# Kernel optimization log

Hardware: AMD Instinct MI355X
Metric: run time of the kernel (lower is better)

## Reference

```python
import jax, jax.numpy as jnp
import numpy as np

EPS = 1e-5
NEG = jnp.float32(-9e15)

def _leaky(z):
    return jnp.where(z >= 0, z, 0.01 * z)

def setup_inputs() -> dict:
    key = jax.random.key(0)
    ks = jax.random.split(key, 12)
    B, N, d_in, d_hid, d_out = 4, 512, 128, 128, 128
    d_mid = d_in // 2
    s = lambda fan: 1.0 / np.sqrt(fan)
    inp = {
        'x': jax.random.normal(ks[0], (B, N, d_in), dtype=jnp.float32),
        'A_init': jax.random.randint(ks[1], (B, N, N), 0, 2, dtype=jnp.int32),
        # Acompute: conv1 (1x1), bn1, conv2 (1x1)
        'W1': jax.random.normal(ks[2], (d_mid, d_in), dtype=jnp.float32) * s(d_in),
        'b1': jnp.zeros((d_mid,), dtype=jnp.float32),
        'g1': jnp.ones((d_mid,), dtype=jnp.float32),
        'be1': jnp.zeros((d_mid,), dtype=jnp.float32),
        'W2': jax.random.normal(ks[3], (1, d_mid), dtype=jnp.float32) * s(d_mid),
        'b2': jnp.zeros((1,), dtype=jnp.float32),
        # Gconv branch1_g0: fc + bn1d
        'Wg': jax.random.normal(ks[4], (d_hid, d_in), dtype=jnp.float32) * s(d_in),
        'bg': jnp.zeros((d_hid,), dtype=jnp.float32),
        'gg': jnp.ones((d_hid,), dtype=jnp.float32),
        'beg': jnp.zeros((d_hid,), dtype=jnp.float32),
        # trans_fc: (d_in + d_hid) -> d_out
        'Wt': jax.random.normal(ks[5], (d_out, d_in + d_hid), dtype=jnp.float32) * s(d_in + d_hid),
        'bt': jnp.zeros((d_out,), dtype=jnp.float32),
    }
    return inp

def reference(x, A_init, W1, b1, g1, be1, W2, b2, Wg, bg, gg, beg, Wt, bt):
    # ---- Acompute: dense pairwise |x_i - x_j| -> 1x1conv -> BN2d -> lrelu -> 1x1conv -> masked softmax
    D = jnp.abs(x[:, :, None, :] - x[:, None, :, :])            # [B, N, N, C]
    h = jnp.einsum('bijc,oc->bijo', D, W1) + b1                 # conv1 (1x1)
    m = jnp.mean(h, axis=(0, 1, 2))                              # BN2d batch stats (training mode)
    v = jnp.mean((h - m) ** 2, axis=(0, 1, 2))                   # biased variance
    h = (h - m) / jnp.sqrt(v + EPS) * g1 + be1
    h = _leaky(h)
    s = jnp.einsum('bijo,uo->biju', h, W2)[..., 0] + b2[0]       # conv2 -> [B, N, N]
    s = jnp.where(A_init > 0, s, NEG)                            # mask non-edges
    A = jax.nn.softmax(s, axis=-1)                               # row-normalized adjacency
    # ---- Gconv branch: bmm -> fc -> BN1d (per-channel over batch*nodes) -> lrelu
    y = jnp.einsum('bij,bjc->bic', A, x)                         # graph aggregation
    y = y @ Wg.T + bg                                            # [B, N, d_hid]
    mg = jnp.mean(y, axis=(0, 1))
    vg = jnp.mean((y - mg) ** 2, axis=(0, 1))
    y = (y - mg) / jnp.sqrt(vg + EPS) * gg + beg
    y = _leaky(y)
    # ---- concat [original, branch1] -> trans_fc
    out = jnp.concatenate([x, y], axis=2) @ Wt.T + bt            # [B, N, d_out]
    return out
```

## Files before the change

### kernel.cpp

```cpp
#include <hip/hip_runtime.h>
#include <hip/hip_bf16.h>
#include <math.h>

#define Bq 4
#define Nq 512
#define Cq 128
#define Oq 64
#define TI 16
#define TJ 8
#define NBLK (Bq*(Nq/TI)*(Nq/TJ))
#define PTOT ((double)Bq*Nq*Nq)
#define NROW (Bq*Nq)
#define EPSq 1e-5f
#define NEGq -9e15f

typedef _Float16 half8 __attribute__((ext_vector_type(8)));
typedef float f32x4 __attribute__((ext_vector_type(4)));

#define OFF_S       0u
#define OFF_YAGG    4194304u
#define OFF_YFC     5242880u
#define OFF_WGT     6291456u
#define OFF_WTT     6356992u
#define OFF_WF      6488064u
#define OFF_PART1   6504448u
#define OFF_RED1    10698752u
#define OFF_SC1     10699776u
#define OFF_PARTG   10700288u
#define OFF_SCG     10962432u
#define WS_NEED     10963456u

__device__ __forceinline__ float lrelu(float v) { return v >= 0.0f ? v : 0.01f * v; }

template <int MODE>
__global__ __launch_bounds__(256, 3) void k_pair_mfma(
    const float* __restrict__ x, const _Float16* __restrict__ Wf,
    const int* __restrict__ A_init, const float* __restrict__ W2,
    const float* __restrict__ b2, const float* __restrict__ scsh,
    float* __restrict__ partial1, float* __restrict__ s_buf) {
  __shared__ float XI[TI][136];
  __shared__ float XJ[TJ][136];
  __shared__ float ep[4][2][64];
  __shared__ float ssc[128];

  const int t = threadIdx.x;
  const int l = t & 63;
  const int wv = __builtin_amdgcn_readfirstlane(t >> 6);
  const int jt = blockIdx.x, it = blockIdx.y, b = blockIdx.z;
  const int i0 = it * TI, j0 = jt * TJ;
  const float* xb = x + (size_t)b * Nq * Cq;

  half8 bf[16];
#pragma unroll
  for (int i = 0; i < 16; ++i)
    bf[i] = *(const half8*)&Wf[(size_t)(i * 64 + l) * 8];

  {
    const int row = t >> 4, col = (t & 15) * 8;
    const float* src = xb + (size_t)(i0 + row) * Cq + col;
    *(float4*)&XI[row][col] = *(const float4*)src;
    *(float4*)&XI[row][col + 4] = *(const float4*)(src + 4);
    if (t < 128) {
      const int rj = t >> 4;
      const float* sj = xb + (size_t)(j0 + rj) * Cq + col;
      *(float4*)&XJ[rj][col] = *(const float4*)sj;
      *(float4*)&XJ[rj][col + 4] = *(const float4*)(sj + 4);
    }
  }
  __syncthreads();

  const int g = l >> 4;
  const int cL = l & 15;
  const int jlan = l & 7;
  const int ilh = (l >> 3) & 1;

  f32x4 zero;
  zero[0] = 0.0f; zero[1] = 0.0f; zero[2] = 0.0f; zero[3] = 0.0f;
  f32x4 acc[2][4];
#pragma unroll
  for (int m = 0; m < 2; ++m)
#pragma unroll
    for (int n = 0; n < 4; ++n) acc[m][n] = zero;

#pragma unroll
  for (int ks = 0; ks < 4; ++ks) {
#pragma unroll
    for (int m = 0; m < 2; ++m) {
      const int mt = wv * 2 + m;
      const int il = mt * 2 + ilh;
      const int c0 = ks * 32 + 4 * g;
      const float4 a0 = *(const float4*)&XI[il][c0];
      const float4 a1 = *(const float4*)&XI[il][c0 + 16];
      const float4 v0 = *(const float4*)&XJ[jlan][c0];
      const float4 v1 = *(const float4*)&XJ[jlan][c0 + 16];
      half8 af;
      af[0] = (_Float16)fabsf(a0.x - v0.x);
      af[1] = (_Float16)fabsf(a0.y - v0.y);
      af[2] = (_Float16)fabsf(a0.z - v0.z);
      af[3] = (_Float16)fabsf(a0.w - v0.w);
      af[4] = (_Float16)fabsf(a1.x - v1.x);
      af[5] = (_Float16)fabsf(a1.y - v1.y);
      af[6] = (_Float16)fabsf(a1.z - v1.z);
      af[7] = (_Float16)fabsf(a1.w - v1.w);
#pragma unroll
      for (int n = 0; n < 4; ++n)
        acc[m][n] = __builtin_amdgcn_mfma_f32_16x16x32_f16(af, bf[ks * 4 + n],
                                                           acc[m][n], 0, 0, 0);
    }
  }

  const int blk = ((b * (Nq / TI) + it) * (Nq / TJ) + jt);

  if (MODE == 0) {
#pragma unroll
    for (int n = 0; n < 4; ++n) {
      float a = 0.0f, q = 0.0f;
#pragma unroll
      for (int m = 0; m < 2; ++m)
#pragma unroll
        for (int r = 0; r < 4; ++r) {
          const float v = acc[m][n][r];
          a += v;
          q += v * v;
        }
      a += __shfl_xor(a, 16); a += __shfl_xor(a, 32);
      q += __shfl_xor(q, 16); q += __shfl_xor(q, 32);
      if (l < 16) {
        ep[wv][0][n * 16 + l] = a;
        ep[wv][1][n * 16 + l] = q;
      }
    }
    __syncthreads();
    if (t < 128) {
      const int o = t & 63, typ = t >> 6;
      const float v = ep[0][typ][o] + ep[1][typ][o] + ep[2][typ][o] + ep[3][typ][o];
      partial1[(size_t)blk * 128 + typ * 64 + o] = v;
    }
    return;
  }

  float sc[4], sh[4], w2[4];
#pragma unroll
  for (int n = 0; n < 4; ++n) {
    const int o = n * 16 + cL;
    sc[n] = scsh[o];
    sh[n] = scsh[64 + o];
    w2[n] = W2[o];
  }
  float sp[2][4];
#pragma unroll
  for (int m = 0; m < 2; ++m)
#pragma unroll
    for (int r = 0; r < 4; ++r) {
      float v = 0.0f;
#pragma unroll
      for (int n = 0; n < 4; ++n) {
        float h = fmaf(acc[m][n][r], sc[n], sh[n]);
        h = lrelu(h);
        v = fmaf(w2[n], h, v);
      }
      v += __shfl_xor(v, 1);
      v += __shfl_xor(v, 2);
      v += __shfl_xor(v, 4);
      v += __shfl_xor(v, 8);
      sp[m][r] = v;
    }
  if (cL == 0) {
#pragma unroll
    for (int m = 0; m < 2; ++m)
#pragma unroll
      for (int r = 0; r < 4; ++r) ssc[wv * 32 + m * 16 + 4 * g + r] = sp[m][r];
  }
  __syncthreads();
  if (t < 128) {
    const int il2 = t >> 3, jl2 = t & 7;
    const size_t arow = ((size_t)b * Nq + (i0 + il2)) * Nq + (j0 + jl2);
    s_buf[arow] = (A_init[arow] > 0) ? ssc[t] + b2[0] : NEGq;
  }
}

__global__ __launch_bounds__(256) void k_reduce1(const float* __restrict__ partial1,
                                                 double* __restrict__ red1) {
  __shared__ double sh[256];
  const int vi = blockIdx.x;
  const int t = threadIdx.x;
  double a = 0.0;
  for (int blk = t; blk < NBLK; blk += 256) a += (double)partial1[(size_t)blk * 128 + vi];
  sh[t] = a;
  __syncthreads();
  for (int off = 128; off > 0; off >>= 1) {
    if (t < off) sh[t] += sh[t + off];
    __syncthreads();
  }
  if (t == 0) red1[vi] = sh[0];
}

__global__ void k_finalize1(const double* __restrict__ red1, const float* __restrict__ g1,
                            const float* __restrict__ be1, float* __restrict__ scsh) {
  const int o = threadIdx.x;
  const double m_raw = red1[o] / PTOT;
  double var = red1[64 + o] / PTOT - m_raw * m_raw;
  if (var < 0.0) var = 0.0;
  const float scale = g1[o] / sqrtf((float)var + EPSq);
  scsh[o] = scale;
  scsh[64 + o] = be1[o] - (float)m_raw * scale;
}

__global__ __launch_bounds__(256) void k_softmax(float* __restrict__ s) {
  __shared__ float r1[4];
  const size_t row = blockIdx.x;
  float* p = s + row * Nq;
  const int t = threadIdx.x;
  float2 v = *(float2*)&p[t * 2];
  float mx = fmaxf(v.x, v.y);
#pragma unroll
  for (int off = 32; off > 0; off >>= 1) mx = fmaxf(mx, __shfl_xor(mx, off));
  if ((t & 63) == 0) r1[t >> 6] = mx;
  __syncthreads();
  mx = fmaxf(fmaxf(r1[0], r1[1]), fmaxf(r1[2], r1[3]));
  const float e0 = expf(v.x - mx), e1 = expf(v.y - mx);
  float ss = e0 + e1;
#pragma unroll
  for (int off = 32; off > 0; off >>= 1) ss += __shfl_xor(ss, off);
  __syncthreads();
  if ((t & 63) == 0) r1[t >> 6] = ss;
  __syncthreads();
  const float tot = r1[0] + r1[1] + r1[2] + r1[3];
  float2 o2;
  o2.x = e0 / tot;
  o2.y = e1 / tot;
  *(float2*)&p[t * 2] = o2;
}

__global__ __launch_bounds__(128) void k_yagg(const float* __restrict__ A,
                                              const float* __restrict__ x,
                                              float* __restrict__ y) {
  const int r0 = blockIdx.x * 4;
  const int b = r0 >> 9;
  const int t = threadIdx.x;
  const float* xb = x + (size_t)b * Nq * Cq + t;
  const float* Ar = A + (size_t)r0 * Nq;
  float acc0 = 0.0f, acc1 = 0.0f, acc2 = 0.0f, acc3 = 0.0f;
#pragma unroll 2
  for (int j = 0; j < Nq; j += 4) {
    const float4 c0 = *(const float4*)&Ar[j];
    const float4 c1 = *(const float4*)&Ar[Nq + j];
    const float4 c2 = *(const float4*)&Ar[2 * Nq + j];
    const float4 c3 = *(const float4*)&Ar[3 * Nq + j];
    const float x0 = xb[(size_t)j * Cq];
    const float x1 = xb[(size_t)(j + 1) * Cq];
    const float x2 = xb[(size_t)(j + 2) * Cq];
    const float x3 = xb[(size_t)(j + 3) * Cq];
    acc0 = fmaf(c0.x, x0, acc0); acc0 = fmaf(c0.y, x1, acc0);
    acc0 = fmaf(c0.z, x2, acc0); acc0 = fmaf(c0.w, x3, acc0);
    acc1 = fmaf(c1.x, x0, acc1); acc1 = fmaf(c1.y, x1, acc1);
    acc1 = fmaf(c1.z, x2, acc1); acc1 = fmaf(c1.w, x3, acc1);
    acc2 = fmaf(c2.x, x0, acc2); acc2 = fmaf(c2.y, x1, acc2);
    acc2 = fmaf(c2.z, x2, acc2); acc2 = fmaf(c2.w, x3, acc2);
    acc3 = fmaf(c3.x, x0, acc3); acc3 = fmaf(c3.y, x1, acc3);
    acc3 = fmaf(c3.z, x2, acc3); acc3 = fmaf(c3.w, x3, acc3);
  }
  y[(size_t)(r0 + 0) * Cq + t] = acc0;
  y[(size_t)(r0 + 1) * Cq + t] = acc1;
  y[(size_t)(r0 + 2) * Cq + t] = acc2;
  y[(size_t)(r0 + 3) * Cq + t] = acc3;
}

__global__ __launch_bounds__(256) void k_yfc(const float* __restrict__ y,
                                             const float* __restrict__ WgT,
                                             const float* __restrict__ bg,
                                             float* __restrict__ yfc,
                                             float* __restrict__ partialg) {
  __shared__ float Y[8][128];
  __shared__ float red[2][8][128];
  const int n0 = blockIdx.x * 8;
  const int t = threadIdx.x;
  const int r = t >> 5, c4 = (t & 31) * 4;
  *(float4*)&Y[r][c4] = *(const float4*)&y[(size_t)(n0 + r) * 128 + c4];
  __syncthreads();
  const float4 bv = *(const float4*)&bg[c4];
  float a0 = bv.x, a1 = bv.y, a2 = bv.z, a3 = bv.w;
#pragma unroll 4
  for (int c = 0; c < 128; ++c) {
    const float yv = Y[r][c];
    const float4 w = *(const float4*)&WgT[(size_t)c * 128 + c4];
    a0 = fmaf(yv, w.x, a0);
    a1 = fmaf(yv, w.y, a1);
    a2 = fmaf(yv, w.z, a2);
    a3 = fmaf(yv, w.w, a3);
  }
  *(float4*)&yfc[(size_t)(n0 + r) * 128 + c4] = make_float4(a0, a1, a2, a3);
  red[0][r][c4] = a0; red[0][r][c4 + 1] = a1; red[0][r][c4 + 2] = a2; red[0][r][c4 + 3] = a3;
  red[1][r][c4] = a0 * a0; red[1][r][c4 + 1] = a1 * a1;
  red[1][r][c4 + 2] = a2 * a2; red[1][r][c4 + 3] = a3 * a3;
  __syncthreads();
  if (t < 128) {
    float s = 0.0f, q = 0.0f;
#pragma unroll
    for (int rr = 0; rr < 8; ++rr) { s += red[0][rr][t]; q += red[1][rr][t]; }
    partialg[(size_t)blockIdx.x * 256 + t] = s;
    partialg[(size_t)blockIdx.x * 256 + 128 + t] = q;
  }
}

__global__ void k_finalizeg(const float* __restrict__ partialg, const float* __restrict__ gg,
                            const float* __restrict__ beg, float* __restrict__ scg) {
  const int h = threadIdx.x;
  double s = 0.0, q = 0.0;
  for (int blk = 0; blk < 256; ++blk) {
    s += (double)partialg[(size_t)blk * 256 + h];
    q += (double)partialg[(size_t)blk * 256 + 128 + h];
  }
  const double m = s / (double)NROW;
  double var = q / (double)NROW - m * m;
  if (var < 0.0) var = 0.0;
  const float scale = gg[h] / sqrtf((float)var + EPSq);
  scg[h] = scale;
  scg[128 + h] = beg[h] - (float)m * scale;
}

__global__ __launch_bounds__(256) void k_out(const float* __restrict__ x,
                                             const float* __restrict__ yfc,
                                             const float* __restrict__ WtT,
                                             const float* __restrict__ bt,
                                             const float* __restrict__ scg,
                                             float* __restrict__ out) {
  __shared__ float XZ[8][256];
  const int n0 = blockIdx.x * 8;
  const int t = threadIdx.x;
  const int r = t >> 5, c4 = (t & 31) * 4;
  *(float4*)&XZ[r][c4] = *(const float4*)&x[(size_t)(n0 + r) * 128 + c4];
  {
    const float4 yv = *(const float4*)&yfc[(size_t)(n0 + r) * 128 + c4];
    const float4 s0 = *(const float4*)&scg[c4];
    const float4 s1 = *(const float4*)&scg[128 + c4];
    XZ[r][128 + c4 + 0] = lrelu(fmaf(yv.x, s0.x, s1.x));
    XZ[r][128 + c4 + 1] = lrelu(fmaf(yv.y, s0.y, s1.y));
    XZ[r][128 + c4 + 2] = lrelu(fmaf(yv.z, s0.z, s1.z));
    XZ[r][128 + c4 + 3] = lrelu(fmaf(yv.w, s0.w, s1.w));
  }
  __syncthreads();
  const float4 bv = *(const float4*)&bt[c4];
  float a0 = bv.x, a1 = bv.y, a2 = bv.z, a3 = bv.w;
#pragma unroll 4
  for (int c = 0; c < 256; ++c) {
    const float xv = XZ[r][c];
    const float4 w = *(const float4*)&WtT[(size_t)c * 128 + c4];
    a0 = fmaf(xv, w.x, a0);
    a1 = fmaf(xv, w.y, a1);
    a2 = fmaf(xv, w.z, a2);
    a3 = fmaf(xv, w.w, a3);
  }
  *(float4*)&out[(size_t)(n0 + r) * 128 + c4] = make_float4(a0, a1, a2, a3);
}

__global__ void k_prep(const float* __restrict__ Wg, const float* __restrict__ Wt,
                       const float* __restrict__ W1, float* __restrict__ WgT,
                       float* __restrict__ WtT, _Float16* __restrict__ Wf) {
  const int idx = blockIdx.x * 256 + threadIdx.x;
  if (idx < 16384) {
    const int h = idx >> 7, c = idx & 127;
    WgT[(size_t)c * 128 + h] = Wg[idx];
  } else if (idx < 49152) {
    const int k2 = idx - 16384;
    const int o = k2 >> 8, k = k2 & 255;
    WtT[(size_t)k * 128 + o] = Wt[k2];
  } else if (idx < 57344) {
    const int f = idx - 49152;
    const int e = f & 7, lane = (f >> 3) & 63, nt = (f >> 9) & 3, ks = f >> 11;
    const int k = ks * 32 + 4 * (lane >> 4) + ((e < 4) ? e : (12 + e));
    const int o = nt * 16 + (lane & 15);
    Wf[f] = (_Float16)W1[o * 128 + k];
  }
}

extern "C" void kernel_launch(void* const* d_in, const int* in_sizes, int n_in,
                              void* d_out, int out_size, void* d_ws, size_t ws_size,
                              hipStream_t stream) {
  const float* x = (const float*)d_in[0];
  const int* A_init = (const int*)d_in[1];
  const float* W1 = (const float*)d_in[2];
  const float* g1 = (const float*)d_in[4];
  const float* be1 = (const float*)d_in[5];
  const float* W2 = (const float*)d_in[6];
  const float* b2 = (const float*)d_in[7];
  const float* Wg = (const float*)d_in[8];
  const float* bg = (const float*)d_in[9];
  const float* gg = (const float*)d_in[10];
  const float* beg = (const float*)d_in[11];
  const float* Wt = (const float*)d_in[12];
  const float* bt = (const float*)d_in[13];
  float* out = (float*)d_out;

  char* ws = (char*)d_ws;
  if (ws_size < WS_NEED) return;
  float* sA = (float*)(ws + OFF_S);
  float* yagg = (float*)(ws + OFF_YAGG);
  float* yfc = (float*)(ws + OFF_YFC);
  float* WgT = (float*)(ws + OFF_WGT);
  float* WtT = (float*)(ws + OFF_WTT);
  _Float16* Wf = (_Float16*)(ws + OFF_WF);
  float* partial1 = (float*)(ws + OFF_PART1);
  double* red1 = (double*)(ws + OFF_RED1);
  float* scsh1 = (float*)(ws + OFF_SC1);
  float* partialg = (float*)(ws + OFF_PARTG);
  float* scg = (float*)(ws + OFF_SCG);

  k_prep<<<224, 256, 0, stream>>>(Wg, Wt, W1, WgT, WtT, Wf);

  dim3 gpass(Nq / TJ, Nq / TI, Bq);
  k_pair_mfma<0><<<gpass, 256, 0, stream>>>(x, Wf, A_init, W2, b2, scsh1, partial1, sA);
  k_reduce1<<<128, 256, 0, stream>>>(partial1, red1);
  k_finalize1<<<1, 64, 0, stream>>>(red1, g1, be1, scsh1);
  k_pair_mfma<1><<<gpass, 256, 0, stream>>>(x, Wf, A_init, W2, b2, scsh1, partial1, sA);
  k_softmax<<<NROW, 256, 0, stream>>>(sA);
  k_yagg<<<NROW / 4, 128, 0, stream>>>(sA, x, yagg);
  k_yfc<<<NROW / 8, 256, 0, stream>>>(yagg, WgT, bg, yfc, partialg);
  k_finalizeg<<<1, 128, 0, stream>>>(partialg, gg, beg, scg);
  k_out<<<NROW / 8, 256, 0, stream>>>(x, yfc, WtT, bt, scg, out);
}
```

Before: 234.2 us.

## Fuse BN stats reduce/finalize, split yagg over j, widen yfc/out blocks

Merges the first BatchNorm reduction and finalize kernels into one kernel that reduces sum and sum-of-squares in float and computes scale/shift directly, removing one launch. k_yagg now splits the j range across two halves of a 256-thread block and combines them through shared memory. k_yfc and k_out use 512 threads, each computing two outputs instead of four, to raise parallelism. The MFMA kernel loads weights as float4 and pins them with an empty asm barrier so the loads are issued before the main loop. Float accumulation of the BN statistics replaces the double-precision reduction, which adds some rounding risk.

```diff
diff --git a/kernel.cpp b/kernel.cpp
--- a/kernel.cpp
+++ b/kernel.cpp
@@ -50,10 +50,10 @@
   const int i0 = it * TI, j0 = jt * TJ;
   const float* xb = x + (size_t)b * Nq * Cq;
 
-  half8 bf[16];
+  float4 bfr[16];
 #pragma unroll
   for (int i = 0; i < 16; ++i)
-    bf[i] = *(const half8*)&Wf[(size_t)(i * 64 + l) * 8];
+    bfr[i] = *(const float4*)&Wf[(size_t)(i * 64 + l) * 8];
 
   {
     const int row = t >> 4, col = (t & 15) * 8;
@@ -68,6 +68,10 @@
     }
   }
   __syncthreads();
+
+#pragma unroll
+  for (int i = 0; i < 16; ++i)
+    asm volatile("" : "+v"(bfr[i].x), "+v"(bfr[i].y), "+v"(bfr[i].z), "+v"(bfr[i].w));
 
   const int g = l >> 4;
   const int cL = l & 15;
@@ -104,8 +108,8 @@
       af[7] = (_Float16)fabsf(a1.w - v1.w);
 #pragma unroll
       for (int n = 0; n < 4; ++n)
-        acc[m][n] = __builtin_amdgcn_mfma_f32_16x16x32_f16(af, bf[ks * 4 + n],
-                                                           acc[m][n], 0, 0, 0);
+        acc[m][n] = __builtin_amdgcn_mfma_f32_16x16x32_f16(
+            af, __builtin_bit_cast(half8, bfr[ks * 4 + n]), acc[m][n], 0, 0, 0);
     }
   }
 
@@ -179,31 +183,36 @@
   }
 }
 
-__global__ __launch_bounds__(256) void k_reduce1(const float* __restrict__ partial1,
-                                                 double* __restrict__ red1) {
-  __shared__ double sh[256];
-  const int vi = blockIdx.x;
-  const int t = threadIdx.x;
-  double a = 0.0;
-  for (int blk = t; blk < NBLK; blk += 256) a += (double)partial1[(size_t)blk * 128 + vi];
-  sh[t] = a;
+__global__ __launch_bounds__(256) void k_stats1(const float* __restrict__ partial1,
+                                                const float* __restrict__ g1,
+                                                const float* __restrict__ be1,
+                                                float* __restrict__ scsh) {
+  __shared__ float sh[2][256];
+  const int o = blockIdx.x;
+  const int t = threadIdx.x;
+  float s = 0.0f, q = 0.0f;
+  for (int blk = t; blk < NBLK; blk += 256) {
+    s += partial1[(size_t)blk * 128 + o];
+    q += partial1[(size_t)blk * 128 + 64 + o];
+  }
+  sh[0][t] = s;
+  sh[1][t] = q;
   __syncthreads();
   for (int off = 128; off > 0; off >>= 1) {
-    if (t < off) sh[t] += sh[t + off];
+    if (t < off) {
+      sh[0][t] += sh[0][t + off];
+      sh[1][t] += sh[1][t + off];
+    }
     __syncthreads();
   }
-  if (t == 0) red1[vi] = sh[0];
-}
-
-__global__ void k_finalize1(const double* __restrict__ red1, const float* __restrict__ g1,
-                            const float* __restrict__ be1, float* __restrict__ scsh) {
-  const int o = threadIdx.x;
-  const double m_raw = red1[o] / PTOT;
-  double var = red1[64 + o] / PTOT - m_raw * m_raw;
-  if (var < 0.0) var = 0.0;
-  const float scale = g1[o] / sqrtf((float)var + EPSq);
-  scsh[o] = scale;
-  scsh[64 + o] = be1[o] - (float)m_raw * scale;
+  if (t == 0) {
+    const double m_raw = (double)sh[0][0] / PTOT;
+    double var = (double)sh[1][0] / PTOT - m_raw * m_raw;
+    if (var < 0.0) var = 0.0;
+    const float scale = g1[o] / sqrtf((float)var + EPSq);
+    scsh[o] = scale;
+    scsh[64 + o] = be1[o] - (float)m_raw * scale;
+  }
 }
 
 __global__ __launch_bounds__(256) void k_softmax(float* __restrict__ s) {
@@ -232,17 +241,19 @@
   *(float2*)&p[t * 2] = o2;
 }
 
-__global__ __launch_bounds__(128) void k_yagg(const float* __restrict__ A,
+__global__ __launch_bounds__(256) void k_yagg(const float* __restrict__ A,
                                               const float* __restrict__ x,
                                               float* __restrict__ y) {
+  __shared__ float red[4][128];
   const int r0 = blockIdx.x * 4;
   const int b = r0 >> 9;
   const int t = threadIdx.x;
-  const float* xb = x + (size_t)b * Nq * Cq + t;
-  const float* Ar = A + (size_t)r0 * Nq;
-  float acc0 = 0.0f, acc1 = 0.0f, acc2 = 0.0f, acc3 = 0.0f;
+  const int hf = t >> 7, c = t & 127;
+  const float* xb = x + (size_t)b * Nq * Cq + (size_t)hf * 256 * Cq + c;
+  const float* Ar = A + (size_t)r0 * Nq + hf * 256;
+  float a0 = 0.0f, a1 = 0.0f, a2 = 0.0f, a3 = 0.0f;
 #pragma unroll 2
-  for (int j = 0; j < Nq; j += 4) {
+  for (int j = 0; j < 256; j += 4) {
     const float4 c0 = *(const float4*)&Ar[j];
     const float4 c1 = *(const float4*)&Ar[Nq + j];
     const float4 c2 = *(const float4*)&Ar[2 * Nq + j];
@@ -251,55 +262,63 @@
     const float x1 = xb[(size_t)(j + 1) * Cq];
     const float x2 = xb[(size_t)(j + 2) * Cq];
     const float x3 = xb[(size_t)(j + 3) * Cq];
-    acc0 = fmaf(c0.x, x0, acc0); acc0 = fmaf(c0.y, x1, acc0);
-    acc0 = fmaf(c0.z, x2, acc0); acc0 = fmaf(c0.w, x3, acc0);
-    acc1 = fmaf(c1.x, x0, acc1); acc1 = fmaf(c1.y, x1, acc1);
-    acc1 = fmaf(c1.z, x2, acc1); acc1 = fmaf(c1.w, x3, acc1);
-    acc2 = fmaf(c2.x, x0, acc2); acc2 = fmaf(c2.y, x1, acc2);
-    acc2 = fmaf(c2.z, x2, acc2); acc2 = fmaf(c2.w, x3, acc2);
-    acc3 = fmaf(c3.x, x0, acc3); acc3 = fmaf(c3.y, x1, acc3);
-    acc3 = fmaf(c3.z, x2, acc3); acc3 = fmaf(c3.w, x3, acc3);
-  }
-  y[(size_t)(r0 + 0) * Cq + t] = acc0;
-  y[(size_t)(r0 + 1) * Cq + t] = acc1;
-  y[(size_t)(r0 + 2) * Cq + t] = acc2;
-  y[(size_t)(r0 + 3) * Cq + t] = acc3;
-}
-
-__global__ __launch_bounds__(256) void k_yfc(const float* __restrict__ y,
+    a0 = fmaf(c0.x, x0, a0); a0 = fmaf(c0.y, x1, a0);
+    a0 = fmaf(c0.z, x2, a0); a0 = fmaf(c0.w, x3, a0);
+    a1 = fmaf(c1.x, x0, a1); a1 = fmaf(c1.y, x1, a1);
+    a1 = fmaf(c1.z, x2, a1); a1 = fmaf(c1.w, x3, a1);
+    a2 = fmaf(c2.x, x0, a2); a2 = fmaf(c2.y, x1, a2);
+    a2 = fmaf(c2.z, x2, a2); a2 = fmaf(c2.w, x3, a2);
+    a3 = fmaf(c3.x, x0, a3); a3 = fmaf(c3.y, x1, a3);
+    a3 = fmaf(c3.z, x2, a3); a3 = fmaf(c3.w, x3, a3);
+  }
+  if (hf) {
+    red[0][c] = a0; red[1][c] = a1; red[2][c] = a2; red[3][c] = a3;
+  }
+  __syncthreads();
+  if (!hf) {
+    y[(size_t)(r0 + 0) * Cq + c] = a0 + red[0][c];
+    y[(size_t)(r0 + 1) * Cq + c] = a1 + red[1][c];
+    y[(size_t)(r0 + 2) * Cq + c] = a2 + red[2][c];
+    y[(size_t)(r0 + 3) * Cq + c] = a3 + red[3][c];
+  }
+}
+
+__global__ __launch_bounds__(512) void k_yfc(const float* __restrict__ y,
                                              const float* __restrict__ WgT,
                                              const float* __restrict__ bg,
                                              float* __restrict__ yfc,
                                              float* __restrict__ partialg) {
   __shared__ float Y[8][128];
-  __shared__ float red[2][8][128];
+  __shared__ float red[8][128];
   const int n0 = blockIdx.x * 8;
   const int t = threadIdx.x;
-  const int r = t >> 5, c4 = (t & 31) * 4;
-  *(float4*)&Y[r][c4] = *(const float4*)&y[(size_t)(n0 + r) * 128 + c4];
-  __syncthreads();
-  const float4 bv = *(const float4*)&bg[c4];
-  float a0 = bv.x, a1 = bv.y, a2 = bv.z, a3 = bv.w;
+  const int r = t >> 6, c2 = (t & 63) * 2;
+  *(float2*)&Y[r][c2] = *(const float2*)&y[(size_t)(n0 + r) * 128 + c2];
+  __syncthreads();
+  const float2 bv = *(const float2*)&bg[c2];
+  float a0 = bv.x, a1 = bv.y;
 #pragma unroll 4
   for (int c = 0; c < 128; ++c) {
     const float yv = Y[r][c];
-    const float4 w = *(const float4*)&WgT[(size_t)c * 128 + c4];
+    const float2 w = *(const float2*)&WgT[(size_t)c * 128 + c2];
     a0 = fmaf(yv, w.x, a0);
     a1 = fmaf(yv, w.y, a1);
-    a2 = fmaf(yv, w.z, a2);
-    a3 = fmaf(yv, w.w, a3);
-  }
-  *(float4*)&yfc[(size_t)(n0 + r) * 128 + c4] = make_float4(a0, a1, a2, a3);
-  red[0][r][c4] = a0; red[0][r][c4 + 1] = a1; red[0][r][c4 + 2] = a2; red[0][r][c4 + 3] = a3;
-  red[1][r][c4] = a0 * a0; red[1][r][c4 + 1] = a1 * a1;
-  red[1][r][c4 + 2] = a2 * a2; red[1][r][c4 + 3] = a3 * a3;
-  __syncthreads();
-  if (t < 128) {
-    float s = 0.0f, q = 0.0f;
-#pragma unroll
-    for (int rr = 0; rr < 8; ++rr) { s += red[0][rr][t]; q += red[1][rr][t]; }
-    partialg[(size_t)blockIdx.x * 256 + t] = s;
-    partialg[(size_t)blockIdx.x * 256 + 128 + t] = q;
+  }
+  *(float2*)&yfc[(size_t)(n0 + r) * 128 + c2] = make_float2(a0, a1);
+  red[r][c2] = a0;
+  red[r][c2 + 1] = a1;
+  __syncthreads();
+  if (t < 256) {
+    const int ch = t & 127, typ = t >> 7;
+    float v = 0.0f;
+    if (typ == 0) {
+#pragma unroll
+      for (int rr = 0; rr < 8; ++rr) v += red[rr][ch];
+    } else {
+#pragma unroll
+      for (int rr = 0; rr < 8; ++rr) v += red[rr][ch] * red[rr][ch];
+    }
+    partialg[(size_t)blockIdx.x * 256 + typ * 128 + ch] = v;
   }
 }
 
@@ -319,7 +338,7 @@
   scg[128 + h] = beg[h] - (float)m * scale;
 }
 
-__global__ __launch_bounds__(256) void k_out(const float* __restrict__ x,
+__global__ __launch_bounds__(512) void k_out(const float* __restrict__ x,
                                              const float* __restrict__ yfc,
                                              const float* __restrict__ WtT,
                                              const float* __restrict__ bt,
@@ -328,30 +347,26 @@
   __shared__ float XZ[8][256];
   const int n0 = blockIdx.x * 8;
   const int t = threadIdx.x;
-  const int r = t >> 5, c4 = (t & 31) * 4;
-  *(float4*)&XZ[r][c4] = *(const float4*)&x[(size_t)(n0 + r) * 128 + c4];
+  const int r = t >> 6, c2 = (t & 63) * 2;
+  *(float2*)&XZ[r][c2] = *(const float2*)&x[(size_t)(n0 + r) * 128 + c2];
   {
-    const float4 yv = *(const float4*)&yfc[(size_t)(n0 + r) * 128 + c4];
-    const float4 s0 = *(const float4*)&scg[c4];
-    const float4 s1 = *(const float4*)&scg[128 + c4];
-    XZ[r][128 + c4 + 0] = lrelu(fmaf(yv.x, s0.x, s1.x));
-    XZ[r][128 + c4 + 1] = lrelu(fmaf(yv.y, s0.y, s1.y));
-    XZ[r][128 + c4 + 2] = lrelu(fmaf(yv.z, s0.z, s1.z));
-    XZ[r][128 + c4 + 3] = lrelu(fmaf(yv.w, s0.w, s1.w));
-  }
-  __syncthreads();
-  const float4 bv = *(const float4*)&bt[c4];
-  float a0 = bv.x, a1 = bv.y, a2 = bv.z, a3 = bv.w;
+    const float2 yv = *(const float2*)&yfc[(size_t)(n0 + r) * 128 + c2];
+    const float2 s0 = *(const float2*)&scg[c2];
+    const float2 s1 = *(const float2*)&scg[128 + c2];
+    XZ[r][128 + c2 + 0] = lrelu(fmaf(yv.x, s0.x, s1.x));
+    XZ[r][128 + c2 + 1] = lrelu(fmaf(yv.y, s0.y, s1.y));
+  }
+  __syncthreads();
+  const float2 bv = *(const float2*)&bt[c2];
+  float a0 = bv.x, a1 = bv.y;
 #pragma unroll 4
   for (int c = 0; c < 256; ++c) {
     const float xv = XZ[r][c];
-    const float4 w = *(const float4*)&WtT[(size_t)c * 128 + c4];
+    const float2 w = *(const float2*)&WtT[(size_t)c * 128 + c2];
     a0 = fmaf(xv, w.x, a0);
     a1 = fmaf(xv, w.y, a1);
-    a2 = fmaf(xv, w.z, a2);
-    a3 = fmaf(xv, w.w, a3);
-  }
-  *(float4*)&out[(size_t)(n0 + r) * 128 + c4] = make_float4(a0, a1, a2, a3);
+  }
+  *(float2*)&out[(size_t)(n0 + r) * 128 + c2] = make_float2(a0, a1);
 }
 
 __global__ void k_prep(const float* __restrict__ Wg, const float* __restrict__ Wt,
@@ -401,7 +416,6 @@
   float* WtT = (float*)(ws + OFF_WTT);
   _Float16* Wf = (_Float16*)(ws + OFF_WF);
   float* partial1 = (float*)(ws + OFF_PART1);
-  double* red1 = (double*)(ws + OFF_RED1);
   float* scsh1 = (float*)(ws + OFF_SC1);
   float* partialg = (float*)(ws + OFF_PARTG);
   float* scg = (float*)(ws + OFF_SCG);
@@ -410,12 +424,11 @@
 
   dim3 gpass(Nq / TJ, Nq / TI, Bq);
   k_pair_mfma<0><<<gpass, 256, 0, stream>>>(x, Wf, A_init, W2, b2, scsh1, partial1, sA);
-  k_reduce1<<<128, 256, 0, stream>>>(partial1, red1);
-  k_finalize1<<<1, 64, 0, stream>>>(red1, g1, be1, scsh1);
+  k_stats1<<<64, 256, 0, stream>>>(partial1, g1, be1, scsh1);
   k_pair_mfma<1><<<gpass, 256, 0, stream>>>(x, Wf, A_init, W2, b2, scsh1, partial1, sA);
   k_softmax<<<NROW, 256, 0, stream>>>(sA);
-  k_yagg<<<NROW / 4, 128, 0, stream>>>(sA, x, yagg);
-  k_yfc<<<NROW / 8, 256, 0, stream>>>(yagg, WgT, bg, yfc, partialg);
+  k_yagg<<<NROW / 4, 256, 0, stream>>>(sA, x, yagg);
+  k_yfc<<<NROW / 8, 512, 0, stream>>>(yagg, WgT, bg, yfc, partialg);
   k_finalizeg<<<1, 128, 0, stream>>>(partialg, gg, beg, scg);
-  k_out<<<NROW / 8, 256, 0, stream>>>(x, yfc, WtT, bt, scg, out);
-}
+  k_out<<<NROW / 8, 512, 0, stream>>>(x, yfc, WtT, bt, scg, out);
+}
```

After: 236.1 us. No clear change (+0.8%).
